# Kernel optimization log

Measured on AMD Instinct MI355X. Metric: run time of the kernel, lower is better.

## Reference

```python
import jax, jax.numpy as jnp
import numpy as np

HIDDEN = 4096
NUM_HEADS = 32
NUM_KV_HEADS = 8
HEAD_DIM = 128
EPS = 1e-6
ROPE_THETA = 1000000.0
T = 2048


def setup_inputs() -> dict:
    key = jax.random.key(0)
    k1, k2, k3, k4, k5 = jax.random.split(key, 5)
    q_size = NUM_HEADS * HEAD_DIM
    kv_size = NUM_KV_HEADS * HEAD_DIM
    return {
        "positions": jnp.arange(T, dtype=jnp.int32),
        "hidden_states": jax.random.normal(k1, (T, HIDDEN), dtype=jnp.float32),
        "w_qkv": jax.random.normal(k2, (HIDDEN, q_size + 2 * kv_size), dtype=jnp.float32) * 0.02,
        "w_o": jax.random.normal(k3, (q_size, HIDDEN), dtype=jnp.float32) * 0.02,
        "q_norm_w": jnp.ones((HEAD_DIM,), dtype=jnp.float32) + 0.01 * jax.random.normal(k4, (HEAD_DIM,), dtype=jnp.float32),
        "k_norm_w": jnp.ones((HEAD_DIM,), dtype=jnp.float32) + 0.01 * jax.random.normal(k5, (HEAD_DIM,), dtype=jnp.float32),
    }


def _rms_norm(x, w, eps=EPS):
    # x: [..., head_dim], normalize over last dim
    var = jnp.mean(jnp.square(x), axis=-1, keepdims=True)
    return x * jax.lax.rsqrt(var + eps) * w


def _apply_rope(x, positions):
    # neox-style rotate-half RoPE, rotary_dim == head_dim
    d = x.shape[-1]
    inv_freq = 1.0 / (ROPE_THETA ** (jnp.arange(0, d, 2, dtype=jnp.float32) / d))
    freqs = positions.astype(jnp.float32)[:, None] * inv_freq[None, :]  # [T, d/2]
    cos = jnp.cos(freqs)[:, None, :]  # [T, 1, d/2]
    sin = jnp.sin(freqs)[:, None, :]
    x1, x2 = jnp.split(x, 2, axis=-1)
    return jnp.concatenate([x1 * cos - x2 * sin, x2 * cos + x1 * sin], axis=-1)


def reference(positions, hidden_states, w_qkv, w_o, q_norm_w, k_norm_w):
    num_tokens = hidden_states.shape[0]
    q_size = NUM_HEADS * HEAD_DIM
    kv_size = NUM_KV_HEADS * HEAD_DIM
    group = NUM_HEADS // NUM_KV_HEADS

    qkv = hidden_states @ w_qkv  # [T, q+2kv]
    q = qkv[:, :q_size].reshape(num_tokens, NUM_HEADS, HEAD_DIM)
    k = qkv[:, q_size:q_size + kv_size].reshape(num_tokens, NUM_KV_HEADS, HEAD_DIM)
    v = qkv[:, q_size + kv_size:].reshape(num_tokens, NUM_KV_HEADS, HEAD_DIM)

    q = _rms_norm(q, q_norm_w)
    k = _rms_norm(k, k_norm_w)
    q = _apply_rope(q, positions)
    k = _apply_rope(k, positions)

    scale = HEAD_DIM ** -0.5
    # GQA: group query heads over shared kv heads
    qg = q.reshape(num_tokens, NUM_KV_HEADS, group, HEAD_DIM)
    scores = jnp.einsum("tkgd,skd->kgts", qg * scale, k)  # [KH, G, T, S]
    causal = positions[:, None] >= positions[None, :]  # [T, S]
    scores = jnp.where(causal[None, None, :, :], scores, jnp.finfo(scores.dtype).min)
    probs = jax.nn.softmax(scores, axis=-1)
    out = jnp.einsum("kgts,skd->tkgd", probs, v)  # [T, KH, G, D]
    out = out.reshape(num_tokens, q_size)
    return out @ w_o
```

## Files before the change

### kernel.cpp

```cpp
#include <hip/hip_runtime.h>
#include <cstdint>
#include <cstddef>

#define T_TOK 2048
#define HID   4096
#define NQH   32
#define NKVH  8
#define HD    128
#define QKV_N 6144

typedef __bf16 bf16x8 __attribute__((ext_vector_type(8)));
typedef __bf16 bf16x4 __attribute__((ext_vector_type(4)));
typedef float  f32x4  __attribute__((ext_vector_type(4)));
typedef float  f32x16 __attribute__((ext_vector_type(16)));

#define AS1 __attribute__((address_space(1)))
#define AS3 __attribute__((address_space(3)))

__device__ __forceinline__ void gll16(const void* g, void* l) {
  __builtin_amdgcn_global_load_lds((const AS1 void*)g, (AS3 void*)l, 16, 0, 0);
}

__global__ __launch_bounds__(256) void k_convert(const float* __restrict__ in,
                                                 __bf16* __restrict__ out, int n4) {
  int i = blockIdx.x * 256 + threadIdx.x;
  if (i >= n4) return;
  float4 v = ((const float4*)in)[i];
  bf16x4 o;
  o[0] = (__bf16)v.x; o[1] = (__bf16)v.y; o[2] = (__bf16)v.z; o[3] = (__bf16)v.w;
  ((bf16x4*)out)[i] = o;
}

__global__ __launch_bounds__(256) void k_transpose(const float* __restrict__ in,
                                                   __bf16* __restrict__ out,
                                                   int R, int C) {
  __shared__ float tile[32][33];
  int c0 = blockIdx.x * 32, r0 = blockIdx.y * 32;
  int tx = threadIdx.x, ty = threadIdx.y;
#pragma unroll
  for (int k = 0; k < 4; ++k)
    tile[ty + k*8][tx] = in[(size_t)(r0 + ty + k*8) * C + c0 + tx];
  __syncthreads();
#pragma unroll
  for (int k = 0; k < 4; ++k)
    out[(size_t)(c0 + ty + k*8) * R + r0 + tx] = (__bf16)tile[tx][ty + k*8];
}

template <int NBNX>
__global__ __launch_bounds__(512, 2) void k_gemm8(const __bf16* __restrict__ A,
                                                  const __bf16* __restrict__ Bt,
                                                  float* __restrict__ C,
                                                  int N, int K) {
  __shared__ alignas(16) char ldsb[131072];
  const int tid = threadIdx.x;
  const int lane = tid & 63, w = tid >> 6;
  const int l16 = lane & 15, lg = lane >> 4;
  const int wm = w >> 2, wn = w & 3;

  const int x = blockIdx.x & 7, idx = blockIdx.x >> 3;
  const int bm = (x & 1) * 4 + (idx & 3);
  const int bn = (x >> 1) * NBNX + (idx >> 2);

  const __bf16* asrc[2];
  const __bf16* bsrc[2];
#pragma unroll
  for (int j = 0; j < 2; ++j) {
    int c = (w * 2 + j) * 64 + lane;
    int r = c >> 2;
    int co = ((c & 3) ^ ((r >> 1) & 3)) * 8;
    asrc[j] = A + (size_t)(bm * 256 + r) * K + co;
    bsrc[j] = Bt + (size_t)(bn * 256 + r) * K + co;
  }
  const int dst0 = w * 2048;

#define RA(buf, mk) (ldsb + (buf) * 65536 + (mk) * 16384)
#define RB(buf, mk) (ldsb + (buf) * 65536 + 32768 + (mk) * 16384)
#define STG_A(buf, mk, kk) { gll16(asrc[0] + (kk) + (mk) * 32, RA(buf, mk) + dst0); \
                             gll16(asrc[1] + (kk) + (mk) * 32, RA(buf, mk) + dst0 + 1024); }
#define STG_B(buf, mk, kk) { gll16(bsrc[0] + (kk) + (mk) * 32, RB(buf, mk) + dst0); \
                             gll16(bsrc[1] + (kk) + (mk) * 32, RB(buf, mk) + dst0 + 1024); }
#define FRAG(base, row) (*(const bf16x8*)((base) + (row) * 64 + ((lg ^ (((row) >> 1) & 3)) << 4)))

  f32x4 acc[8][4] = {};
  const int nkt = K >> 6;

  STG_A(0, 0, 0); STG_B(0, 0, 0); STG_A(0, 1, 0); STG_B(0, 1, 0);

  for (int t = 0; t < nkt - 1; ++t) {
    const int cur = t & 1, nxt = cur ^ 1;
    const int kn = (t + 1) * 64;
    bf16x8 a0[4], a1[4], b0[4];

    STG_A(nxt, 0, kn);
    asm volatile("s_waitcnt vmcnt(6)" ::: "memory");
    __builtin_amdgcn_s_barrier();
    __builtin_amdgcn_sched_barrier(0);
#pragma unroll
    for (int i = 0; i < 4; ++i) a0[i] = FRAG(RA(cur, 0), wm * 128 + i * 16 + l16);
#pragma unroll
    for (int n = 0; n < 4; ++n) b0[n] = FRAG(RB(cur, 0), wn * 64 + n * 16 + l16);
    __builtin_amdgcn_s_setprio(1);
#pragma unroll
    for (int i = 0; i < 4; ++i)
#pragma unroll
      for (int n = 0; n < 4; ++n)
        acc[i][n] = __builtin_amdgcn_mfma_f32_16x16x32_bf16(a0[i], b0[n], acc[i][n], 0, 0, 0);
    __builtin_amdgcn_s_setprio(0);
    __builtin_amdgcn_s_barrier();

#pragma unroll
    for (int i = 0; i < 4; ++i) a1[i] = FRAG(RA(cur, 0), wm * 128 + 64 + i * 16 + l16);
    STG_B(nxt, 0, kn);
    __builtin_amdgcn_s_barrier();
    __builtin_amdgcn_s_setprio(1);
#pragma unroll
    for (int i = 0; i < 4; ++i)
#pragma unroll
      for (int n = 0; n < 4; ++n)
        acc[4 + i][n] = __builtin_amdgcn_mfma_f32_16x16x32_bf16(a1[i], b0[n], acc[4 + i][n], 0, 0, 0);
    __builtin_amdgcn_s_setprio(0);
    __builtin_amdgcn_s_barrier();

    STG_A(nxt, 1, kn);
    asm volatile("s_waitcnt vmcnt(6)" ::: "memory");
    __builtin_amdgcn_s_barrier();
    __builtin_amdgcn_sched_barrier(0);
#pragma unroll
    for (int i = 0; i < 4; ++i) a0[i] = FRAG(RA(cur, 1), wm * 128 + i * 16 + l16);
#pragma unroll
    for (int n = 0; n < 4; ++n) b0[n] = FRAG(RB(cur, 1), wn * 64 + n * 16 + l16);
    __builtin_amdgcn_s_setprio(1);
#pragma unroll
    for (int i = 0; i < 4; ++i)
#pragma unroll
      for (int n = 0; n < 4; ++n)
        acc[i][n] = __builtin_amdgcn_mfma_f32_16x16x32_bf16(a0[i], b0[n], acc[i][n], 0, 0, 0);
    __builtin_amdgcn_s_setprio(0);
    __builtin_amdgcn_s_barrier();

#pragma unroll
    for (int i = 0; i < 4; ++i) a1[i] = FRAG(RA(cur, 1), wm * 128 + 64 + i * 16 + l16);
    STG_B(nxt, 1, kn);
    __builtin_amdgcn_s_barrier();
    __builtin_amdgcn_s_setprio(1);
#pragma unroll
    for (int i = 0; i < 4; ++i)
#pragma unroll
      for (int n = 0; n < 4; ++n)
        acc[4 + i][n] = __builtin_amdgcn_mfma_f32_16x16x32_bf16(a1[i], b0[n], acc[4 + i][n], 0, 0, 0);
    __builtin_amdgcn_s_setprio(0);
    __builtin_amdgcn_s_barrier();
  }

  asm volatile("s_waitcnt vmcnt(0)" ::: "memory");
  __builtin_amdgcn_s_barrier();
  __builtin_amdgcn_sched_barrier(0);
  {
    const int cur = (nkt - 1) & 1;
#pragma unroll
    for (int mk = 0; mk < 2; ++mk) {
      bf16x8 aa[8], bb[4];
#pragma unroll
      for (int i = 0; i < 8; ++i) aa[i] = FRAG(RA(cur, mk), wm * 128 + i * 16 + l16);
#pragma unroll
      for (int n = 0; n < 4; ++n) bb[n] = FRAG(RB(cur, mk), wn * 64 + n * 16 + l16);
#pragma unroll
      for (int i = 0; i < 8; ++i)
#pragma unroll
        for (int n = 0; n < 4; ++n)
          acc[i][n] = __builtin_amdgcn_mfma_f32_16x16x32_bf16(aa[i], bb[n], acc[i][n], 0, 0, 0);
    }
  }
#undef RA
#undef RB
#undef STG_A
#undef STG_B
#undef FRAG

#pragma unroll
  for (int mi = 0; mi < 8; ++mi)
#pragma unroll
    for (int ni = 0; ni < 4; ++ni) {
      int row = bm * 256 + wm * 128 + mi * 16 + lg * 4;
      int col = bn * 256 + wn * 64 + ni * 16 + l16;
#pragma unroll
      for (int r = 0; r < 4; ++r)
        C[(size_t)(row + r) * N + col] = acc[mi][ni][r];
    }
}

__global__ __launch_bounds__(64) void k_norm_rope(const float* __restrict__ qkv,
                                                  const int* __restrict__ pos,
                                                  const float* __restrict__ qw,
                                                  const float* __restrict__ kw,
                                                  __bf16* __restrict__ qo,
                                                  __bf16* __restrict__ ko,
                                                  __bf16* __restrict__ vto) {
  const int slot = blockIdx.x;
  const int t    = blockIdx.y;
  const int i    = threadIdx.x;
  const int off  = (slot < 32) ? slot * 128
                 : (slot < 40) ? 4096 + (slot - 32) * 128
                                : 5120 + (slot - 40) * 128;
  const float* base = qkv + (size_t)t * QKV_N + off;
  float x1 = base[i], x2 = base[i + 64];
  if (slot >= 40) {
    __bf16* o = vto + ((size_t)(slot - 40) * HD) * T_TOK + t;
    o[(size_t)i * T_TOK] = (__bf16)x1;
    o[(size_t)(i + 64) * T_TOK] = (__bf16)x2;
    return;
  }
  float ss = x1 * x1 + x2 * x2;
#pragma unroll
  for (int m = 32; m >= 1; m >>= 1) ss += __shfl_xor(ss, m);
  float rinv = rsqrtf(ss * (1.0f / 128.0f) + 1e-6f);
  const float* wn = (slot < 32) ? qw : kw;
  float n1 = x1 * rinv * wn[i];
  float n2 = x2 * rinv * wn[i + 64];
  float fr = (float)pos[t] * expf((float)i * -0.21586735246819178f);
  float cs = cosf(fr), sn = sinf(fr);
  float o1 = n1 * cs - n2 * sn;
  float o2 = n2 * cs + n1 * sn;
  if (slot < 32) {
    const float QSC = 0.08838834764831845f * 1.4426950408889634f;
    __bf16* o = qo + ((size_t)t * NQH + slot) * HD;
    o[i] = (__bf16)(o1 * QSC);
    o[i + 64] = (__bf16)(o2 * QSC);
  } else {
    __bf16* o = ko + ((size_t)t * NKVH + (slot - 32)) * HD;
    o[i] = (__bf16)o1;
    o[i + 64] = (__bf16)o2;
  }
}

__global__ __launch_bounds__(256, 2) void k_attn(const __bf16* __restrict__ Q,
                                                 const __bf16* __restrict__ K,
                                                 const __bf16* __restrict__ Vt,
                                                 __bf16* __restrict__ O) {
  __shared__ alignas(16) __bf16 Ks[64 * 128];
  __shared__ alignas(16) __bf16 Vts[128 * 64];
  const int bid = blockIdx.x;
  const int kvh = bid & 7;
  const int qc  = bid >> 3;
  const int tid = threadIdx.x, lane = tid & 63, w = tid >> 6;
  const int l31 = lane & 31, hi = lane >> 5;
  const int h  = kvh * 4 + w;
  const int q0 = qc * 32;
  const int qrow = q0 + l31;
  char* Ksb = (char*)Ks;
  char* Vtb = (char*)Vts;

  bf16x8 qf[8];
  {
    const __bf16* qp = Q + ((size_t)qrow * NQH + h) * HD + hi * 8;
#pragma unroll
    for (int dc = 0; dc < 8; ++dc)
      qf[dc] = *(const bf16x8*)(qp + dc * 16);
  }

  size_t ksrc[4], vsrc[4];
#pragma unroll
  for (int j = 0; j < 4; ++j) {
    int kr = w * 16 + j * 4 + (lane >> 4);
    ksrc[j] = ((size_t)kr * NKVH + kvh) * HD + (size_t)(((lane & 15) ^ (kr & 15)) * 8);
    int vr = w * 32 + j * 8 + (lane >> 3);
    vsrc[j] = ((size_t)(kvh * HD + vr)) * T_TOK + (size_t)(((lane & 7) ^ (vr & 7)) * 8);
  }

  float m_run = -3.0e38f, l_run = 0.f;
  f32x16 ot[4] = {};

  const int ntiles = (qc >> 1) + 1;
  for (int tt = 0; tt < ntiles; ++tt) {
    const int s0 = tt * 64;
#pragma unroll
    for (int j = 0; j < 4; ++j) {
      gll16(K + (size_t)s0 * (NKVH * HD) + ksrc[j], Ksb + (w * 4 + j) * 1024);
      gll16(Vt + (size_t)s0 + vsrc[j], Vtb + (w * 4 + j) * 1024);
    }
    __syncthreads();

    f32x16 sac[2] = {};
#pragma unroll
    for (int hf = 0; hf < 2; ++hf) {
      int krow = hf * 32 + l31;
#pragma unroll
      for (int dc = 0; dc < 8; ++dc) {
        bf16x8 kf = *(const bf16x8*)(Ksb + krow * 256 + (((dc * 2 + hi) ^ (krow & 15)) * 16));
        sac[hf] = __builtin_amdgcn_mfma_f32_32x32x16_bf16(kf, qf[dc], sac[hf], 0, 0, 0);
      }
    }

    float pv[32];
    if (s0 + 64 > q0) {
#pragma unroll
      for (int hf = 0; hf < 2; ++hf)
#pragma unroll
        for (int r = 0; r < 16; ++r) {
          int kvg = s0 + hf * 32 + (r & 3) + ((r >> 2) * 8) + hi * 4;
          pv[hf * 16 + r] = (kvg > qrow) ? -3.0e38f : sac[hf][r];
        }
    } else {
#pragma unroll
      for (int hf = 0; hf < 2; ++hf)
#pragma unroll
        for (int r = 0; r < 16; ++r) pv[hf * 16 + r] = sac[hf][r];
    }
    float t16[16];
#pragma unroll
    for (int i = 0; i < 16; ++i) t16[i] = fmaxf(pv[i], pv[i + 16]);
#pragma unroll
    for (int i = 0; i < 8; ++i) t16[i] = fmaxf(t16[i], t16[i + 8]);
#pragma unroll
    for (int i = 0; i < 4; ++i) t16[i] = fmaxf(t16[i], t16[i + 4]);
    float mt = fmaxf(fmaxf(t16[0], t16[1]), fmaxf(t16[2], t16[3]));
    mt = fmaxf(mt, __shfl_xor(mt, 32));
    if (!__all(mt - m_run <= 10.0f)) {
      float m_new = fmaxf(m_run, mt);
      float corr = exp2f(m_run - m_new);
      l_run *= corr;
#pragma unroll
      for (int dt = 0; dt < 4; ++dt)
#pragma unroll
        for (int r = 0; r < 16; ++r) ot[dt][r] *= corr;
      m_run = m_new;
    }
#pragma unroll
    for (int i = 0; i < 32; ++i) pv[i] = exp2f(pv[i] - m_run);
#pragma unroll
    for (int i = 0; i < 16; ++i) t16[i] = pv[i] + pv[i + 16];
#pragma unroll
    for (int i = 0; i < 8; ++i) t16[i] += t16[i + 8];
#pragma unroll
    for (int i = 0; i < 4; ++i) t16[i] += t16[i + 4];
    float rs = (t16[0] + t16[1]) + (t16[2] + t16[3]);
    rs += __shfl_xor(rs, 32);
    l_run += rs;

    uint32_t wds[16];
#pragma unroll
    for (int i = 0; i < 16; ++i) {
      uint32_t r;
      asm("v_cvt_pk_bf16_f32 %0, %1, %2" : "=v"(r) : "v"(pv[2 * i]), "v"(pv[2 * i + 1]));
      wds[i] = r;
    }
#pragma unroll
    for (int c = 0; c < 4; ++c) {
      const int base = (c >> 1) * 8 + (c & 1) * 4;
      uint32_t sa = hi ? wds[base + 0] : wds[base + 2];
      uint32_t sb = hi ? wds[base + 1] : wds[base + 3];
      uint32_t ra = __shfl_xor(sa, 32);
      uint32_t rb = __shfl_xor(sb, 32);
      union { uint32_t u[4]; bf16x8 v; } pf;
      pf.u[0] = hi ? ra : wds[base + 0];
      pf.u[1] = hi ? rb : wds[base + 1];
      pf.u[2] = hi ? wds[base + 2] : ra;
      pf.u[3] = hi ? wds[base + 3] : rb;
#pragma unroll
      for (int dt = 0; dt < 4; ++dt) {
        int vrow = dt * 32 + l31;
        bf16x8 vf = *(const bf16x8*)(Vtb + vrow * 128 + (((c * 2 + hi) ^ (vrow & 7)) * 16));
        ot[dt] = __builtin_amdgcn_mfma_f32_32x32x16_bf16(vf, pf.v, ot[dt], 0, 0, 0);
      }
    }
    __syncthreads();
  }

  float inv = 1.0f / l_run;
  char* Ob = Ksb + w * 8192;
#pragma unroll
  for (int dt = 0; dt < 4; ++dt)
#pragma unroll
    for (int r = 0; r < 16; ++r) {
      int d = dt * 32 + (r & 3) + ((r >> 2) * 8) + hi * 4;
      *(__bf16*)(Ob + l31 * 256 + ((d * 2) ^ ((l31 & 7) << 4))) = (__bf16)(ot[dt][r] * inv);
    }
#pragma unroll
  for (int pass = 0; pass < 8; ++pass) {
    int q = pass * 4 + (lane >> 4);
    int ch = lane & 15;
    bf16x8 vvv = *(const bf16x8*)(Ob + q * 256 + ((ch ^ (q & 7)) * 16));
    *(bf16x8*)(O + ((size_t)(q0 + q) * NQH + h) * HD + ch * 8) = vvv;
  }
}

extern "C" void kernel_launch(void* const* d_in, const int* in_sizes, int n_in,
                              void* d_out, int out_size, void* d_ws, size_t ws_size,
                              hipStream_t stream) {
  const int*   positions = (const int*)d_in[0];
  const float* hidden    = (const float*)d_in[1];
  const float* w_qkv     = (const float*)d_in[2];
  const float* w_o       = (const float*)d_in[3];
  const float* q_norm    = (const float*)d_in[4];
  const float* k_norm    = (const float*)d_in[5];
  float* out = (float*)d_out;

  char* ws = (char*)d_ws;
  __bf16* wqkv_t   = (__bf16*)ws;
  __bf16* wo_t     = (__bf16*)(ws + 50331648);
  __bf16* hidden_b = (__bf16*)(ws + 83886080);
  float*  qkv      = (float*)(ws + 100663296);
  __bf16* qb  = (__bf16*)ws;
  __bf16* kb  = (__bf16*)(ws + 16777216);
  __bf16* vtb = (__bf16*)(ws + 20971520);
  __bf16* attn_o = hidden_b;

  k_convert<<<dim3((T_TOK * HID / 4 + 255) / 256), 256, 0, stream>>>(hidden, hidden_b, T_TOK * HID / 4);
  k_transpose<<<dim3(QKV_N / 32, HID / 32), dim3(32, 8), 0, stream>>>(w_qkv, wqkv_t, HID, QKV_N);
  k_transpose<<<dim3(HID / 32, HID / 32), dim3(32, 8), 0, stream>>>(w_o, wo_t, HID, HID);
  k_gemm8<6><<<dim3(192), 512, 0, stream>>>(hidden_b, wqkv_t, qkv, QKV_N, HID);
  k_norm_rope<<<dim3(48, T_TOK), 64, 0, stream>>>(qkv, positions, q_norm, k_norm, qb, kb, vtb);
  k_attn<<<dim3(512), 256, 0, stream>>>(qb, kb, vtb, attn_o);
  k_gemm8<4><<<dim3(128), 512, 0, stream>>>(attn_o, wo_t, out, HID, HID);
}
```

Before: 361.1 us.

## Shrink GEMM block tiles to 128xN so both GEMMs launch 256 blocks

Reworks the bf16 MFMA GEMM from 256x256 block tiles to 128-row tiles with a templated N width (384 for QKV, 256 for the output projection). Each block now runs 256 blocks instead of 192 or 128, filling the 256 CUs. LDS staging, swizzled loads, wait counts and the per-wave fragment layout are rebuilt to match. Smaller tiles lower per-block arithmetic intensity and add global/L2 traffic.

```diff
diff --git a/kernel.cpp b/kernel.cpp
--- a/kernel.cpp
+++ b/kernel.cpp
@@ -46,42 +46,42 @@
     out[(size_t)(c0 + ty + k*8) * R + r0 + tx] = (__bf16)tile[tx][ty + k*8];
 }
 
-template <int NBNX>
+template <int NFR>
 __global__ __launch_bounds__(512, 2) void k_gemm8(const __bf16* __restrict__ A,
                                                   const __bf16* __restrict__ Bt,
                                                   float* __restrict__ C,
                                                   int N, int K) {
-  __shared__ alignas(16) char ldsb[131072];
+  constexpr int BN   = 64 * NFR;
+  constexpr int WN   = 16 * NFR;
+  constexpr int NB   = NFR / 2;
+  constexpr int NH   = NFR / 2;
+  constexpr int BREG = BN * 64;
+  constexpr int BUFSZ = 16384 + 2 * BREG;
+  __shared__ alignas(16) char ldsb[2 * BUFSZ];
   const int tid = threadIdx.x;
   const int lane = tid & 63, w = tid >> 6;
   const int l16 = lane & 15, lg = lane >> 4;
   const int wm = w >> 2, wn = w & 3;
 
   const int x = blockIdx.x & 7, idx = blockIdx.x >> 3;
-  const int bm = (x & 1) * 4 + (idx & 3);
-  const int bn = (x >> 1) * NBNX + (idx >> 2);
-
-  const __bf16* asrc[2];
-  const __bf16* bsrc[2];
-#pragma unroll
-  for (int j = 0; j < 2; ++j) {
-    int c = (w * 2 + j) * 64 + lane;
-    int r = c >> 2;
-    int co = ((c & 3) ^ ((r >> 1) & 3)) * 8;
-    asrc[j] = A + (size_t)(bm * 256 + r) * K + co;
-    bsrc[j] = Bt + (size_t)(bn * 256 + r) * K + co;
-  }
-  const int dst0 = w * 2048;
-
-#define RA(buf, mk) (ldsb + (buf) * 65536 + (mk) * 16384)
-#define RB(buf, mk) (ldsb + (buf) * 65536 + 32768 + (mk) * 16384)
-#define STG_A(buf, mk, kk) { gll16(asrc[0] + (kk) + (mk) * 32, RA(buf, mk) + dst0); \
-                             gll16(asrc[1] + (kk) + (mk) * 32, RA(buf, mk) + dst0 + 1024); }
-#define STG_B(buf, mk, kk) { gll16(bsrc[0] + (kk) + (mk) * 32, RB(buf, mk) + dst0); \
-                             gll16(bsrc[1] + (kk) + (mk) * 32, RB(buf, mk) + dst0 + 1024); }
+  const int bm = (x & 1) * 8 + (idx & 7);
+  const int bn = (x >> 1) * 4 + (idx >> 3);
+
+  const int rA = tid >> 2, pA = tid & 3;
+  const __bf16* asrc = A + (size_t)(bm * 128 + rA) * K + ((pA ^ ((rA >> 1) & 3)) * 8);
+  const __bf16* bsrc = Bt + (size_t)(bn * BN + rA) * K + ((pA ^ ((rA >> 1) & 3)) * 8);
+
+#define RA_(buf, mk) (ldsb + (buf) * BUFSZ + (mk) * 8192)
+#define RB_(buf, mk) (ldsb + (buf) * BUFSZ + 16384 + (mk) * BREG)
+#define STG_A(buf, mk, kk) { gll16(asrc + (kk) + (mk) * 32, RA_(buf, mk) + w * 1024); }
+#define STG_B(buf, mk, kk) { _Pragma("unroll") \
+    for (int j = 0; j < NB; ++j) \
+      gll16(bsrc + (size_t)j * 128 * K + (kk) + (mk) * 32, RB_(buf, mk) + j * 8192 + w * 1024); }
 #define FRAG(base, row) (*(const bf16x8*)((base) + (row) * 64 + ((lg ^ (((row) >> 1) & 3)) << 4)))
-
-  f32x4 acc[8][4] = {};
+#define WAITN() { if constexpr (NFR == 6) asm volatile("s_waitcnt vmcnt(4)" ::: "memory"); \
+                  else                    asm volatile("s_waitcnt vmcnt(3)" ::: "memory"); }
+
+  f32x4 acc[4][NFR] = {};
   const int nkt = K >> 6;
 
   STG_A(0, 0, 0); STG_B(0, 0, 0); STG_A(0, 1, 0); STG_B(0, 1, 0);
@@ -89,65 +89,65 @@
   for (int t = 0; t < nkt - 1; ++t) {
     const int cur = t & 1, nxt = cur ^ 1;
     const int kn = (t + 1) * 64;
-    bf16x8 a0[4], a1[4], b0[4];
+    bf16x8 af[4], bf_[NH];
 
     STG_A(nxt, 0, kn);
-    asm volatile("s_waitcnt vmcnt(6)" ::: "memory");
+    WAITN();
     __builtin_amdgcn_s_barrier();
     __builtin_amdgcn_sched_barrier(0);
 #pragma unroll
-    for (int i = 0; i < 4; ++i) a0[i] = FRAG(RA(cur, 0), wm * 128 + i * 16 + l16);
-#pragma unroll
-    for (int n = 0; n < 4; ++n) b0[n] = FRAG(RB(cur, 0), wn * 64 + n * 16 + l16);
+    for (int i = 0; i < 4; ++i) af[i] = FRAG(RA_(cur, 0), wm * 64 + i * 16 + l16);
+#pragma unroll
+    for (int n = 0; n < NH; ++n) bf_[n] = FRAG(RB_(cur, 0), wn * WN + n * 16 + l16);
     __builtin_amdgcn_s_setprio(1);
 #pragma unroll
     for (int i = 0; i < 4; ++i)
 #pragma unroll
-      for (int n = 0; n < 4; ++n)
-        acc[i][n] = __builtin_amdgcn_mfma_f32_16x16x32_bf16(a0[i], b0[n], acc[i][n], 0, 0, 0);
+      for (int n = 0; n < NH; ++n)
+        acc[i][n] = __builtin_amdgcn_mfma_f32_16x16x32_bf16(af[i], bf_[n], acc[i][n], 0, 0, 0);
     __builtin_amdgcn_s_setprio(0);
     __builtin_amdgcn_s_barrier();
 
 #pragma unroll
-    for (int i = 0; i < 4; ++i) a1[i] = FRAG(RA(cur, 0), wm * 128 + 64 + i * 16 + l16);
+    for (int n = 0; n < NH; ++n) bf_[n] = FRAG(RB_(cur, 0), wn * WN + (NH + n) * 16 + l16);
     STG_B(nxt, 0, kn);
     __builtin_amdgcn_s_barrier();
     __builtin_amdgcn_s_setprio(1);
 #pragma unroll
     for (int i = 0; i < 4; ++i)
 #pragma unroll
-      for (int n = 0; n < 4; ++n)
-        acc[4 + i][n] = __builtin_amdgcn_mfma_f32_16x16x32_bf16(a1[i], b0[n], acc[4 + i][n], 0, 0, 0);
+      for (int n = 0; n < NH; ++n)
+        acc[i][NH + n] = __builtin_amdgcn_mfma_f32_16x16x32_bf16(af[i], bf_[n], acc[i][NH + n], 0, 0, 0);
     __builtin_amdgcn_s_setprio(0);
     __builtin_amdgcn_s_barrier();
 
     STG_A(nxt, 1, kn);
-    asm volatile("s_waitcnt vmcnt(6)" ::: "memory");
+    WAITN();
     __builtin_amdgcn_s_barrier();
     __builtin_amdgcn_sched_barrier(0);
 #pragma unroll
-    for (int i = 0; i < 4; ++i) a0[i] = FRAG(RA(cur, 1), wm * 128 + i * 16 + l16);
-#pragma unroll
-    for (int n = 0; n < 4; ++n) b0[n] = FRAG(RB(cur, 1), wn * 64 + n * 16 + l16);
+    for (int i = 0; i < 4; ++i) af[i] = FRAG(RA_(cur, 1), wm * 64 + i * 16 + l16);
+#pragma unroll
+    for (int n = 0; n < NH; ++n) bf_[n] = FRAG(RB_(cur, 1), wn * WN + n * 16 + l16);
     __builtin_amdgcn_s_setprio(1);
 #pragma unroll
     for (int i = 0; i < 4; ++i)
 #pragma unroll
-      for (int n = 0; n < 4; ++n)
-        acc[i][n] = __builtin_amdgcn_mfma_f32_16x16x32_bf16(a0[i], b0[n], acc[i][n], 0, 0, 0);
+      for (int n = 0; n < NH; ++n)
+        acc[i][n] = __builtin_amdgcn_mfma_f32_16x16x32_bf16(af[i], bf_[n], acc[i][n], 0, 0, 0);
     __builtin_amdgcn_s_setprio(0);
     __builtin_amdgcn_s_barrier();
 
 #pragma unroll
-    for (int i = 0; i < 4; ++i) a1[i] = FRAG(RA(cur, 1), wm * 128 + 64 + i * 16 + l16);
+    for (int n = 0; n < NH; ++n) bf_[n] = FRAG(RB_(cur, 1), wn * WN + (NH + n) * 16 + l16);
     STG_B(nxt, 1, kn);
     __builtin_amdgcn_s_barrier();
     __builtin_amdgcn_s_setprio(1);
 #pragma unroll
     for (int i = 0; i < 4; ++i)
 #pragma unroll
-      for (int n = 0; n < 4; ++n)
-        acc[4 + i][n] = __builtin_amdgcn_mfma_f32_16x16x32_bf16(a1[i], b0[n], acc[4 + i][n], 0, 0, 0);
+      for (int n = 0; n < NH; ++n)
+        acc[i][NH + n] = __builtin_amdgcn_mfma_f32_16x16x32_bf16(af[i], bf_[n], acc[i][NH + n], 0, 0, 0);
     __builtin_amdgcn_s_setprio(0);
     __builtin_amdgcn_s_barrier();
   }
@@ -159,30 +159,31 @@
     const int cur = (nkt - 1) & 1;
 #pragma unroll
     for (int mk = 0; mk < 2; ++mk) {
-      bf16x8 aa[8], bb[4];
-#pragma unroll
-      for (int i = 0; i < 8; ++i) aa[i] = FRAG(RA(cur, mk), wm * 128 + i * 16 + l16);
-#pragma unroll
-      for (int n = 0; n < 4; ++n) bb[n] = FRAG(RB(cur, mk), wn * 64 + n * 16 + l16);
-#pragma unroll
-      for (int i = 0; i < 8; ++i)
-#pragma unroll
-        for (int n = 0; n < 4; ++n)
+      bf16x8 aa[4], bb[NFR];
+#pragma unroll
+      for (int i = 0; i < 4; ++i) aa[i] = FRAG(RA_(cur, mk), wm * 64 + i * 16 + l16);
+#pragma unroll
+      for (int n = 0; n < NFR; ++n) bb[n] = FRAG(RB_(cur, mk), wn * WN + n * 16 + l16);
+#pragma unroll
+      for (int i = 0; i < 4; ++i)
+#pragma unroll
+        for (int n = 0; n < NFR; ++n)
           acc[i][n] = __builtin_amdgcn_mfma_f32_16x16x32_bf16(aa[i], bb[n], acc[i][n], 0, 0, 0);
     }
   }
-#undef RA
-#undef RB
+#undef RA_
+#undef RB_
 #undef STG_A
 #undef STG_B
 #undef FRAG
-
-#pragma unroll
-  for (int mi = 0; mi < 8; ++mi)
-#pragma unroll
-    for (int ni = 0; ni < 4; ++ni) {
-      int row = bm * 256 + wm * 128 + mi * 16 + lg * 4;
-      int col = bn * 256 + wn * 64 + ni * 16 + l16;
+#undef WAITN
+
+#pragma unroll
+  for (int mi = 0; mi < 4; ++mi)
+#pragma unroll
+    for (int ni = 0; ni < NFR; ++ni) {
+      int row = bm * 128 + wm * 64 + mi * 16 + lg * 4;
+      int col = bn * BN + wn * WN + ni * 16 + l16;
 #pragma unroll
       for (int r = 0; r < 4; ++r)
         C[(size_t)(row + r) * N + col] = acc[mi][ni][r];
@@ -408,8 +409,8 @@
   k_convert<<<dim3((T_TOK * HID / 4 + 255) / 256), 256, 0, stream>>>(hidden, hidden_b, T_TOK * HID / 4);
   k_transpose<<<dim3(QKV_N / 32, HID / 32), dim3(32, 8), 0, stream>>>(w_qkv, wqkv_t, HID, QKV_N);
   k_transpose<<<dim3(HID / 32, HID / 32), dim3(32, 8), 0, stream>>>(w_o, wo_t, HID, HID);
-  k_gemm8<6><<<dim3(192), 512, 0, stream>>>(hidden_b, wqkv_t, qkv, QKV_N, HID);
+  k_gemm8<6><<<dim3(256), 512, 0, stream>>>(hidden_b, wqkv_t, qkv, QKV_N, HID);
   k_norm_rope<<<dim3(48, T_TOK), 64, 0, stream>>>(qkv, positions, q_norm, k_norm, qb, kb, vtb);
   k_attn<<<dim3(512), 256, 0, stream>>>(qb, kb, vtb, attn_o);
-  k_gemm8<4><<<dim3(128), 512, 0, stream>>>(attn_o, wo_t, out, HID, HID);
-}
+  k_gemm8<4><<<dim3(256), 512, 0, stream>>>(attn_o, wo_t, out, HID, HID);
+}
```

Result: faster. 327.9 us (-9.2%).
